# Optimization experiments

Measured on AMD Instinct MI355X. Metric: run time of the kernel, lower is better.

## Reference

```python
import jax, jax.numpy as jnp
import numpy as np

N = 50000      # num nodes
E = 400000     # num edges
D = 128        # embed_size (MLP output size)
H = 256        # MLP hidden size
HOPS = 3       # num_hops


def _mlp_params(key, in_dim):
    k1, k2, k3, k4 = jax.random.split(key, 4)
    u = lambda k, s: jax.random.uniform(k, s, minval=-0.1, maxval=0.1, dtype=jnp.float32)
    return u(k1, (in_dim, H)), u(k2, (H,)), u(k3, (H, D)), u(k4, (D,))


def _mlp(x, W1, b1, W2, b2):
    # Linear -> ReLU -> Linear -> ReLU (Dropout is identity at eval)
    return jax.nn.relu(jax.nn.relu(x @ W1 + b1) @ W2 + b2)


def _scatter_mean(vals, idx, counts):
    s = jax.ops.segment_sum(vals, idx, num_segments=N)
    return s / counts[:, None]


def setup_inputs() -> dict:
    key = jax.random.key(0)
    ks = jax.random.split(key, 14)
    inp = {
        "batch_token": jax.random.normal(ks[0], (N, D), jnp.float32),
        "edge_p_node": jax.random.randint(ks[1], (E,), 0, N),
        "edge_c_node": jax.random.randint(ks[2], (E,), 0, N),
        "edge_p_indicate": jax.random.uniform(ks[3], (E,), jnp.float32),
        "edge_c_indicate": jax.random.uniform(ks[4], (E,), jnp.float32),
        "p_mask": jax.random.uniform(ks[5], (N,), jnp.float32),
        "c_mask": jax.random.uniform(ks[6], (N,), jnp.float32),
        "start_token": jax.random.normal(ks[7], (D,), jnp.float32),
        "end_token": jax.random.normal(ks[8], (D,), jnp.float32),
    }
    for name, kk, in_dim in [("v", ks[9], D), ("e", ks[10], 1), ("p", ks[11], 3 * D),
                             ("c", ks[12], 3 * D), ("a", ks[13], 3 * D)]:
        W1, b1, W2, b2 = _mlp_params(kk, in_dim)
        inp[name + "W1"], inp[name + "b1"], inp[name + "W2"], inp[name + "b2"] = W1, b1, W2, b2
    return inp


def reference(batch_token, edge_p_node, edge_c_node, edge_p_indicate, edge_c_indicate,
              p_mask, c_mask, start_token, end_token,
              vW1, vb1, vW2, vb2, eW1, eb1, eW2, eb2,
              pW1, pb1, pW2, pb2, cW1, cb1, cW2, cb2,
              aW1, ab1, aW2, ab2):
    edge_p = _mlp(edge_p_indicate[:, None], eW1, eb1, eW2, eb2)   # [E, D]
    edge_c = _mlp(edge_c_indicate[:, None], eW1, eb1, eW2, eb2)   # [E, D]
    hidden = _mlp(batch_token, vW1, vb1, vW2, vb2)                # [N, D]

    ones_e = jnp.ones((E,), jnp.float32)
    cnt_p = jnp.maximum(jax.ops.segment_sum(ones_e, edge_p_node, num_segments=N), 1.0)
    cnt_c = jnp.maximum(jax.ops.segment_sum(ones_e, edge_c_node, num_segments=N), 1.0)

    for _ in range(HOPS):
        hp = hidden[edge_p_node]                                  # [E, D]
        hc = hidden[edge_c_node]                                  # [E, D]
        S_p = _mlp(jnp.concatenate([hc, hp, edge_p], -1), pW1, pb1, pW2, pb2)
        S_c = _mlp(jnp.concatenate([hp, hc, edge_c], -1), cW1, cb1, cW2, cb2)
        S_p = _scatter_mean(S_p, edge_p_node, cnt_p) + p_mask[:, None] * start_token
        S_c = _scatter_mean(S_c, edge_c_node, cnt_c) + c_mask[:, None] * end_token
        x_aggr = jnp.concatenate([hidden, S_p, S_c], -1)          # [N, 3D]
        hidden = hidden + _mlp(x_aggr, aW1, ab1, aW2, ab2)
    return hidden
```

## Files before the change

### kernel.cpp

```cpp
#include <hip/hip_runtime.h>
#include <stdint.h>

#define N_NODES 50000
#define N_EDGES 400000
#define M_TAB 4096

typedef short s8v __attribute__((ext_vector_type(8)));
typedef float f4v __attribute__((ext_vector_type(4)));

static __device__ __forceinline__ unsigned short f2bf(float f) {
  union { float f; uint32_t u; } v; v.f = f;
  return (unsigned short)((v.u + 0x7FFFu + ((v.u >> 16) & 1u)) >> 16);
}
static __device__ __forceinline__ ushort4 f2bf4(float4 v) {
  ushort4 o; o.x = f2bf(v.x); o.y = f2bf(v.y); o.z = f2bf(v.z); o.w = f2bf(v.w);
  return o;
}
static __device__ __forceinline__ void bf2(uint32_t u, float& a, float& b) {
  union { uint32_t x; float f; } lo, hi;
  lo.x = u << 16; hi.x = u & 0xffff0000u;
  a = lo.f; b = hi.f;
}
static __device__ __forceinline__ f4v mfma16(s8v a, s8v b, f4v c) {
  return __builtin_amdgcn_mfma_f32_16x16x32_bf16(a, b, c, 0, 0, 0);
}
static __device__ __forceinline__ void gload_lds16(const void* g, void* l) {
  __builtin_amdgcn_global_load_lds(
      (const __attribute__((address_space(1))) uint32_t*)g,
      (__attribute__((address_space(3))) uint32_t*)l, 16, 0, 0);
}

__global__ __launch_bounds__(256) void z_gemm_kernel(
    const float* __restrict__ hid, const unsigned short* __restrict__ Wsw,
    unsigned short* __restrict__ Z)
{
  __shared__ __align__(16) unsigned short B[256 * 128];
  const int tid = threadIdx.x, lane = tid & 63, wv = tid >> 6;
  const int g = blockIdx.y;
  const unsigned short* src = Wsw + (size_t)g * 256 * 128;
#pragma unroll
  for (int it = 0; it < 16; ++it) {
    int q = it * 4 + wv;
    gload_lds16(src + (size_t)q * 512 + lane * 8, &B[q * 512]);
  }
  __syncthreads();
  const int l15 = lane & 15, kg = lane >> 4;
  const f4v vz = {0.f, 0.f, 0.f, 0.f};
  for (int c0 = blockIdx.x; c0 < (N_NODES + 63) / 64; c0 += gridDim.x) {
    const int base = c0 * 64;
    const int row = base + wv * 16 + l15;
    s8v af[4];
#pragma unroll
    for (int k = 0; k < 4; ++k) {
      float4 u0 = {0.f,0.f,0.f,0.f}, u1 = {0.f,0.f,0.f,0.f};
      if (row < N_NODES) {
        u0 = *(const float4*)(hid + (size_t)row * 128 + k * 32 + kg * 8);
        u1 = *(const float4*)(hid + (size_t)row * 128 + k * 32 + kg * 8 + 4);
      }
      s8v a;
      a[0] = (short)f2bf(u0.x); a[1] = (short)f2bf(u0.y);
      a[2] = (short)f2bf(u0.z); a[3] = (short)f2bf(u0.w);
      a[4] = (short)f2bf(u1.x); a[5] = (short)f2bf(u1.y);
      a[6] = (short)f2bf(u1.z); a[7] = (short)f2bf(u1.w);
      af[k] = a;
    }
    f4v acc[16];
#pragma unroll
    for (int t = 0; t < 16; ++t) acc[t] = vz;
#pragma unroll
    for (int k = 0; k < 4; ++k) {
#pragma unroll
      for (int t = 0; t < 16; ++t) {
        int j = t * 16 + l15;
        s8v b = *(const s8v*)(&B[j * 128 + (((k * 4 + kg) ^ (j & 7)) * 8)]);
        acc[t] = mfma16(af[k], b, acc[t]);
      }
    }
#pragma unroll
    for (int t = 0; t < 16; ++t) {
      int c = t * 16 + l15;
#pragma unroll
      for (int j = 0; j < 4; ++j) {
        int ro = base + wv * 16 + kg * 4 + j;
        if (ro < N_NODES) Z[(size_t)ro * 512 + g * 256 + c] = f2bf(acc[t][j]);
      }
    }
  }
}

__global__ __launch_bounds__(256) void tab_gemm_kernel(
    const unsigned short* __restrict__ feat,
    const unsigned short* __restrict__ Wsw,
    const float* __restrict__ b1, unsigned short* __restrict__ T)
{
  __shared__ __align__(16) unsigned short B[256 * 128];
  const int tid = threadIdx.x, lane = tid & 63, wv = tid >> 6;
#pragma unroll
  for (int it = 0; it < 16; ++it) {
    int q = it * 4 + wv;
    gload_lds16(Wsw + (size_t)q * 512 + lane * 8, &B[q * 512]);
  }
  __syncthreads();
  const int l15 = lane & 15, kg = lane >> 4;
  const int base = blockIdx.x * 64;
  const int row = base + wv * 16 + l15;
  s8v af[4];
#pragma unroll
  for (int k = 0; k < 4; ++k)
    af[k] = *(const s8v*)(feat + (size_t)row * 128 + k * 32 + kg * 8);
  const f4v vz = {0.f, 0.f, 0.f, 0.f};
  f4v acc[16];
#pragma unroll
  for (int t = 0; t < 16; ++t) acc[t] = vz;
#pragma unroll
  for (int k = 0; k < 4; ++k) {
#pragma unroll
    for (int t = 0; t < 16; ++t) {
      int j = t * 16 + l15;
      s8v b = *(const s8v*)(&B[j * 128 + (((k * 4 + kg) ^ (j & 7)) * 8)]);
      acc[t] = mfma16(af[k], b, acc[t]);
    }
  }
#pragma unroll
  for (int t = 0; t < 16; ++t) {
    int c = t * 16 + l15;
    float bb = b1[c];
#pragma unroll
    for (int j = 0; j < 4; ++j) {
      int ro = base + wv * 16 + kg * 4 + j;
      T[(size_t)ro * 256 + c] = f2bf(acc[t][j] + bb);
    }
  }
}

__global__ __launch_bounds__(256) void edge_msg3_kernel(
    const unsigned short* __restrict__ Z,
    const float* __restrict__ ind,
    const int* __restrict__ n0idx, const int* __restrict__ n1idx,
    const unsigned short* __restrict__ T,
    const unsigned short* __restrict__ W2stg, const float* __restrict__ b2,
    float* __restrict__ Sacc, const float* __restrict__ rcpv)
{
  __shared__ __align__(16) unsigned short H1[64 * 256];
  __shared__ __align__(16) unsigned short Wb[2][4096];
  __shared__ int n0s[64], n1s[64], tix[64];
  __shared__ float tfr[64];
  const int tid = threadIdx.x, lane = tid & 63, wv = tid >> 6;
  const int l15 = lane & 15, kg = lane >> 4;
  const int base = blockIdx.x * 64;
  if (tid < 64) {
    n0s[tid] = n0idx[base + tid];
    n1s[tid] = n1idx[base + tid];
    float x = ind[base + tid];
    float xs = x * (float)M_TAB;
    int idx = (int)xs;
    idx = idx < 0 ? 0 : (idx > M_TAB - 1 ? M_TAB - 1 : idx);
    tix[tid] = idx;
    tfr[tid] = xs - (float)idx;
  }
#pragma unroll
  for (int i = 0; i < 2; ++i) {
    int q = wv * 2 + i;
    gload_lds16(W2stg + (size_t)q * 512 + lane * 8, &Wb[0][q * 512]);
  }
  __syncthreads();
#pragma unroll
  for (int it = 0; it < 8; ++it) {
    int i = tid + it * 256;
    int r = i >> 5, c8 = i & 31;
    const uint4 za = *(const uint4*)(Z + (size_t)n0s[r] * 512 + c8 * 8);
    const uint4 zb = *(const uint4*)(Z + (size_t)n1s[r] * 512 + 256 + c8 * 8);
    const uint4 t0 = *(const uint4*)(T + (size_t)tix[r] * 256 + c8 * 8);
    const uint4 t1 = *(const uint4*)(T + (size_t)(tix[r] + 1) * 256 + c8 * 8);
    const float f = tfr[r];
    uint32_t ua[4] = {za.x, za.y, za.z, za.w};
    uint32_t ub[4] = {zb.x, zb.y, zb.z, zb.w};
    uint32_t u0[4] = {t0.x, t0.y, t0.z, t0.w};
    uint32_t u1[4] = {t1.x, t1.y, t1.z, t1.w};
    uint32_t uo[4];
#pragma unroll
    for (int q = 0; q < 4; ++q) {
      float a0, a1, b0, b1f, p0, p1, q0, q1;
      bf2(ua[q], a0, a1); bf2(ub[q], b0, b1f);
      bf2(u0[q], p0, p1); bf2(u1[q], q0, q1);
      float s0 = fmaxf(a0 + b0 + p0 + f * (q0 - p0), 0.f);
      float s1 = fmaxf(a1 + b1f + p1 + f * (q1 - p1), 0.f);
      uo[q] = (uint32_t)f2bf(s0) | ((uint32_t)f2bf(s1) << 16);
    }
    uint4 pk; pk.x = uo[0]; pk.y = uo[1]; pk.z = uo[2]; pk.w = uo[3];
    *(uint4*)(H1 + r * 256 + ((c8 ^ (r & 7)) * 8)) = pk;
  }
  __syncthreads();
  const int rr = wv * 16 + l15;
  s8v af2[8];
#pragma unroll
  for (int k = 0; k < 8; ++k)
    af2[k] = *(const s8v*)(H1 + rr * 256 + (((k * 4 + kg) ^ (l15 & 7)) * 8));
  const f4v vz = {0.f, 0.f, 0.f, 0.f};
  f4v acc2[8];
#pragma unroll
  for (int t = 0; t < 8; ++t) acc2[t] = vz;
#pragma unroll
  for (int s = 0; s < 8; ++s) {
    if (s < 7) {
#pragma unroll
      for (int i = 0; i < 2; ++i) {
        int q = wv * 2 + i;
        gload_lds16(W2stg + (size_t)(s + 1) * 4096 + q * 512 + lane * 8,
                    &Wb[(s + 1) & 1][q * 512]);
      }
    }
#pragma unroll
    for (int t = 0; t < 8; ++t) {
      s8v b = *(const s8v*)(&Wb[s & 1][kg * 1024 + (t * 16 + l15) * 8]);
      acc2[t] = mfma16(af2[s], b, acc2[t]);
    }
    __syncthreads();
  }
  int n1r[4]; float tscr[4];
#pragma unroll
  for (int j = 0; j < 4; ++j) {
    int r = wv * 16 + kg * 4 + j;
    int n1 = n1s[r];
    n1r[j] = n1; tscr[j] = rcpv[n1];
  }
#pragma unroll
  for (int t = 0; t < 8; ++t) {
    int c = t * 16 + l15;
    float bb = b2[c];
#pragma unroll
    for (int j = 0; j < 4; ++j) {
      float v = fmaxf(acc2[t][j] + bb, 0.f) * tscr[j];
      atomicAdd(Sacc + (size_t)n1r[j] * 128 + c, v);
    }
  }
}

__global__ __launch_bounds__(256, 2) void aggr_kernel(
    float* __restrict__ hid,
    const float* __restrict__ Sp, const float* __restrict__ Sc,
    const float* __restrict__ pm, const float* __restrict__ cm,
    const float* __restrict__ st, const float* __restrict__ et,
    const unsigned short* __restrict__ W1stg, const float* __restrict__ b1,
    const unsigned short* __restrict__ W2stg, const float* __restrict__ b2)
{
  __shared__ __align__(16) unsigned short ABUF[64 * 384];
  __shared__ __align__(16) unsigned short Wb[2][8192];
  const int tid = threadIdx.x, lane = tid & 63, wv = tid >> 6;
  const int l15 = lane & 15, kg = lane >> 4;
  const int base = blockIdx.x * 64;
#pragma unroll
  for (int i = 0; i < 4; ++i) {
    int q = wv * 4 + i;
    gload_lds16(W1stg + (size_t)q * 512 + lane * 8, &Wb[0][q * 512]);
  }
#pragma unroll
  for (int it = 0; it < 24; ++it) {
    int i = tid + it * 256;
    int r = i / 96, q = i - r * 96;
    int seg = q >> 5, c4 = q & 31;
    int n = base + r;
    float4 v = {0.f, 0.f, 0.f, 0.f};
    if (n < N_NODES) {
      if (seg == 0) {
        v = *(const float4*)(hid + (size_t)n * 128 + c4 * 4);
      } else if (seg == 1) {
        v = *(const float4*)(Sp + (size_t)n * 128 + c4 * 4);
        float m = pm[n]; const float4 t = *(const float4*)(st + c4 * 4);
        v.x = fmaf(m, t.x, v.x); v.y = fmaf(m, t.y, v.y);
        v.z = fmaf(m, t.z, v.z); v.w = fmaf(m, t.w, v.w);
      } else {
        v = *(const float4*)(Sc + (size_t)n * 128 + c4 * 4);
        float m = cm[n]; const float4 t = *(const float4*)(et + c4 * 4);
        v.x = fmaf(m, t.x, v.x); v.y = fmaf(m, t.y, v.y);
        v.z = fmaf(m, t.z, v.z); v.w = fmaf(m, t.w, v.w);
      }
    }
    int unit = seg * 16 + (c4 >> 1);
    *(ushort4*)(ABUF + r * 384 + ((unit ^ (r & 7)) * 8) + (c4 & 1) * 4) = f2bf4(v);
  }
  __syncthreads();
  const int rr = wv * 16 + l15;
  s8v af1[12];
#pragma unroll
  for (int k = 0; k < 12; ++k)
    af1[k] = *(const s8v*)(ABUF + rr * 384 + (((k * 4 + kg) ^ (rr & 7)) * 8));
  const f4v vz = {0.f, 0.f, 0.f, 0.f};
  f4v acc1[16];
#pragma unroll
  for (int t = 0; t < 16; ++t) acc1[t] = vz;
#pragma unroll
  for (int s = 0; s < 12; ++s) {
    if (s < 11) {
#pragma unroll
      for (int i = 0; i < 4; ++i) {
        int q = wv * 4 + i;
        gload_lds16(W1stg + (size_t)(s + 1) * 8192 + q * 512 + lane * 8,
                    &Wb[(s + 1) & 1][q * 512]);
      }
    } else {
#pragma unroll
      for (int i = 0; i < 2; ++i) {
        int q = wv * 2 + i;
        gload_lds16(W2stg + (size_t)q * 512 + lane * 8, &Wb[0][q * 512]);
      }
    }
#pragma unroll
    for (int t = 0; t < 16; ++t) {
      s8v b = *(const s8v*)(&Wb[s & 1][kg * 2048 + (t * 16 + l15) * 8]);
      acc1[t] = mfma16(af1[s], b, acc1[t]);
    }
    __syncthreads();
  }
#pragma unroll
  for (int t = 0; t < 16; ++t) {
    int c = t * 16 + l15;
    float bb = b1[c];
#pragma unroll
    for (int j = 0; j < 4; ++j) {
      int r = wv * 16 + kg * 4 + j;
      ABUF[r * 256 + (((c >> 3) ^ (r & 7)) * 8) + (c & 7)] =
          f2bf(fmaxf(acc1[t][j] + bb, 0.f));
    }
  }
  __syncthreads();
  s8v af2[8];
#pragma unroll
  for (int k = 0; k < 8; ++k)
    af2[k] = *(const s8v*)(ABUF + rr * 256 + (((k * 4 + kg) ^ (l15 & 7)) * 8));
  f4v acc2[8];
#pragma unroll
  for (int t = 0; t < 8; ++t) acc2[t] = vz;
#pragma unroll
  for (int s = 0; s < 8; ++s) {
    if (s < 7) {
#pragma unroll
      for (int i = 0; i < 2; ++i) {
        int q = wv * 2 + i;
        gload_lds16(W2stg + (size_t)(s + 1) * 4096 + q * 512 + lane * 8,
                    &Wb[(s + 1) & 1][q * 512]);
      }
    }
#pragma unroll
    for (int t = 0; t < 8; ++t) {
      s8v b = *(const s8v*)(&Wb[s & 1][kg * 1024 + (t * 16 + l15) * 8]);
      acc2[t] = mfma16(af2[s], b, acc2[t]);
    }
    __syncthreads();
  }
#pragma unroll
  for (int t = 0; t < 8; ++t) {
    int c = t * 16 + l15;
    float bb = b2[c];
#pragma unroll
    for (int j = 0; j < 4; ++j) {
      int ro = base + wv * 16 + kg * 4 + j;
      if (ro < N_NODES) hid[(size_t)ro * 128 + c] += fmaxf(acc2[t][j] + bb, 0.f);
    }
  }
}

__global__ __launch_bounds__(256) void edge_feat_kernel(
    const float* __restrict__ ind, const float* __restrict__ W1,
    const float* __restrict__ b1,
    const unsigned short* __restrict__ W2sw,
    const float* __restrict__ b2, unsigned short* __restrict__ feat,
    int ntiles)
{
  __shared__ __align__(16) unsigned short B[128 * 256];
  __shared__ unsigned short H1[64 * 264];
  __shared__ float xs[64];
  const int tid = threadIdx.x, lane = tid & 63, wv = tid >> 6;
  const int l15 = lane & 15, kg = lane >> 4;
#pragma unroll
  for (int it = 0; it < 16; ++it) {
    int q = it * 4 + wv;
    gload_lds16(W2sw + (size_t)q * 512 + lane * 8, &B[q * 512]);
  }
  const float w = W1[tid], bb1 = b1[tid];
  const f4v vz = {0.f, 0.f, 0.f, 0.f};
  for (int tile = blockIdx.x; tile < ntiles; tile += gridDim.x) {
    const int base = tile * 64;
    if (tid < 64) xs[tid] = ind[base + tid];
    __syncthreads();
    for (int r = 0; r < 64; ++r)
      H1[r * 264 + tid] = f2bf(fmaxf(fmaf(xs[r], w, bb1), 0.f));
    __syncthreads();
    const unsigned short* Hrow = H1 + (size_t)(wv * 16 + l15) * 264;
    s8v af2[8];
#pragma unroll
    for (int k = 0; k < 8; ++k) af2[k] = *(const s8v*)(Hrow + k * 32 + kg * 8);
    f4v acc2[8];
#pragma unroll
    for (int t = 0; t < 8; ++t) acc2[t] = vz;
#pragma unroll
    for (int k = 0; k < 8; ++k) {
#pragma unroll
      for (int t = 0; t < 8; ++t) {
        int j = t * 16 + l15;
        s8v b = *(const s8v*)(&B[j * 256 + (((k * 4 + kg) ^ (j & 7)) * 8)]);
        acc2[t] = mfma16(af2[k], b, acc2[t]);
      }
    }
#pragma unroll
    for (int t = 0; t < 8; ++t) {
      int c = t * 16 + l15;
      float b2c = b2[c];
#pragma unroll
      for (int j = 0; j < 4; ++j) {
        int e = base + wv * 16 + kg * 4 + j;
        feat[(size_t)e * 128 + c] = f2bf(fmaxf(acc2[t][j] + b2c, 0.f));
      }
    }
    __syncthreads();
  }
}

template <int KST1>
static __device__ __forceinline__ void mlp_core(
    unsigned short* __restrict__ BUF,
    const unsigned short* __restrict__ W1t, const float* __restrict__ b1,
    const unsigned short* __restrict__ W2t,
    int l15, int kg, int wr0, f4v* __restrict__ acc2)
{
  const int ldA = KST1 * 32 + 8;
  const f4v vzero = {0.f, 0.f, 0.f, 0.f};
  const unsigned short* Arow = BUF + (size_t)(wr0 + l15) * ldA;
  s8v af1[KST1];
#pragma unroll
  for (int k = 0; k < KST1; ++k) af1[k] = *(const s8v*)(Arow + k * 32 + kg * 8);
  __syncthreads();
  f4v acc1[16];
#pragma unroll
  for (int t = 0; t < 16; ++t) acc1[t] = vzero;
#pragma unroll
  for (int k = 0; k < KST1; ++k) {
#pragma unroll
    for (int t = 0; t < 16; ++t) {
      s8v b = *(const s8v*)(W1t + (size_t)(t * 16 + l15) * (KST1 * 32) + k * 32 + kg * 8);
      acc1[t] = mfma16(af1[k], b, acc1[t]);
    }
  }
#pragma unroll
  for (int t = 0; t < 16; ++t) {
    int c = t * 16 + l15;
    float bb = b1[c];
#pragma unroll
    for (int j = 0; j < 4; ++j) {
      BUF[(size_t)(wr0 + kg * 4 + j) * 264 + c] = f2bf(fmaxf(acc1[t][j] + bb, 0.f));
    }
  }
  const unsigned short* Hrow = BUF + (size_t)(wr0 + l15) * 264;
  s8v af2[8];
#pragma unroll
  for (int k = 0; k < 8; ++k) af2[k] = *(const s8v*)(Hrow + k * 32 + kg * 8);
#pragma unroll
  for (int t = 0; t < 8; ++t) acc2[t] = vzero;
#pragma unroll
  for (int k = 0; k < 8; ++k) {
#pragma unroll
    for (int t = 0; t < 8; ++t) {
      s8v b = *(const s8v*)(W2t + (size_t)(t * 16 + l15) * 256 + k * 32 + kg * 8);
      acc2[t] = mfma16(af2[k], b, acc2[t]);
    }
  }
}

__global__ __launch_bounds__(256, 2) void v_mlp_kernel(
    const float* __restrict__ x,
    const unsigned short* __restrict__ W1t, const float* __restrict__ b1,
    const unsigned short* __restrict__ W2t, const float* __restrict__ b2,
    float* __restrict__ hid)
{
  __shared__ unsigned short BUF[64 * 264];
  const int tid = threadIdx.x;
  const int base = blockIdx.x * 64;
#pragma unroll
  for (int it = 0; it < 8; ++it) {
    int i = tid + it * 256;
    int r = i >> 5, c4 = i & 31, n = base + r;
    float4 v = {0.f, 0.f, 0.f, 0.f};
    if (n < N_NODES) v = *(const float4*)(x + (size_t)n * 128 + c4 * 4);
    *(ushort4*)(BUF + r * 136 + c4 * 4) = f2bf4(v);
  }
  __syncthreads();
  const int lane = tid & 63, wv = tid >> 6;
  const int l15 = lane & 15, kg = lane >> 4, wr0 = wv * 16;
  f4v acc2[8];
  mlp_core<4>(BUF, W1t, b1, W2t, l15, kg, wr0, acc2);
#pragma unroll
  for (int t = 0; t < 8; ++t) {
    int c = t * 16 + l15;
    float bb = b2[c];
#pragma unroll
    for (int j = 0; j < 4; ++j) {
      int n = base + wr0 + kg * 4 + j;
      if (n < N_NODES) hid[(size_t)n * 128 + c] = fmaxf(acc2[t][j] + bb, 0.f);
    }
  }
}

__global__ void transpose_w(const float* __restrict__ W, unsigned short* __restrict__ Wt,
                            int K, int NH) {
  int i = blockIdx.x * 256 + threadIdx.x;
  if (i < K * NH) {
    int k = i / NH, n = i - k * NH;
    Wt[(size_t)n * K + k] = f2bf(W[i]);
  }
}

__global__ void build_w1stg(const float* __restrict__ W, unsigned short* __restrict__ stg) {
  int i = blockIdx.x * 256 + threadIdx.x;
  if (i < 384 * 256) {
    int k = i >> 8, out = i & 255;
    int s = k >> 5, kc = (k >> 3) & 3, j = k & 7;
    stg[(size_t)s * 8192 + kc * 2048 + out * 8 + j] = f2bf(W[i]);
  }
}

__global__ void build_w2stg(const float* __restrict__ W, unsigned short* __restrict__ stg) {
  int i = blockIdx.x * 256 + threadIdx.x;
  if (i < 256 * 128) {
    int k = i >> 7, out = i & 127;
    int s = k >> 5, kc = (k >> 3) & 3, j = k & 7;
    stg[(size_t)s * 4096 + kc * 1024 + out * 8 + j] = f2bf(W[i]);
  }
}

__global__ void build_w128_sw(const float* __restrict__ W, int k_off,
                              unsigned short* __restrict__ dst) {
  int i = blockIdx.x * 256 + threadIdx.x;
  if (i < 256 * 128) {
    int j = i >> 7, e = i & 127;
    int unit = (e >> 3) ^ (j & 7);
    dst[(size_t)j * 128 + unit * 8 + (e & 7)] = f2bf(W[(size_t)(k_off + e) * 256 + j]);
  }
}

__global__ void build_w2sw(const float* __restrict__ W, unsigned short* __restrict__ dst) {
  int i = blockIdx.x * 256 + threadIdx.x;
  if (i < 128 * 256) {
    int j = i >> 8, k = i & 255;
    dst[(size_t)j * 256 + (((k >> 3) ^ (j & 7)) * 8) + (k & 7)] =
        f2bf(W[(size_t)k * 128 + j]);
  }
}

__global__ void make_samples(float* __restrict__ xs) {
  int i = blockIdx.x * 256 + threadIdx.x;
  if (i < 4160) {
    int s = i < M_TAB ? i : M_TAB;
    xs[i] = (float)s * (1.f / (float)M_TAB);
  }
}

__global__ void count_kernel(const int* __restrict__ pn, const int* __restrict__ cn,
                             float* __restrict__ cp, float* __restrict__ cc) {
  int i = blockIdx.x * 256 + threadIdx.x;
  if (i < N_EDGES) {
    atomicAdd(cp + pn[i], 1.f);
    atomicAdd(cc + cn[i], 1.f);
  }
}

__global__ void rcp_kernel(float* __restrict__ cp, float* __restrict__ cc) {
  int i = blockIdx.x * 256 + threadIdx.x;
  if (i < N_NODES) {
    cp[i] = 1.f / fmaxf(cp[i], 1.f);
    cc[i] = 1.f / fmaxf(cc[i], 1.f);
  }
}

extern "C" void kernel_launch(void* const* d_in, const int* in_sizes, int n_in,
                              void* d_out, int out_size, void* d_ws, size_t ws_size,
                              hipStream_t stream) {
  const float* batch_token = (const float*)d_in[0];
  const int*   pn          = (const int*)d_in[1];
  const int*   cn          = (const int*)d_in[2];
  const float* indP        = (const float*)d_in[3];
  const float* indC        = (const float*)d_in[4];
  const float* p_mask      = (const float*)d_in[5];
  const float* c_mask      = (const float*)d_in[6];
  const float* stok        = (const float*)d_in[7];
  const float* etok        = (const float*)d_in[8];
  const float* vW1 = (const float*)d_in[9],  *vb1 = (const float*)d_in[10];
  const float* vW2 = (const float*)d_in[11], *vb2 = (const float*)d_in[12];
  const float* eW1 = (const float*)d_in[13], *eb1 = (const float*)d_in[14];
  const float* eW2 = (const float*)d_in[15], *eb2 = (const float*)d_in[16];
  const float* pW1 = (const float*)d_in[17], *pb1 = (const float*)d_in[18];
  const float* pW2 = (const float*)d_in[19], *pb2 = (const float*)d_in[20];
  const float* cW1 = (const float*)d_in[21], *cb1 = (const float*)d_in[22];
  const float* cW2 = (const float*)d_in[23], *cb2 = (const float*)d_in[24];
  const float* aW1 = (const float*)d_in[25], *ab1 = (const float*)d_in[26];
  const float* aW2 = (const float*)d_in[27], *ab2 = (const float*)d_in[28];

  char* w = (char*)d_ws;
  auto alloc = [&](size_t bytes) -> char* {
    char* p = w;
    w += (bytes + 255) & ~(size_t)255;
    return p;
  };
  float* Sp    = (float*)alloc((size_t)N_NODES * 128 * 4);
  float* Sc    = (float*)alloc((size_t)N_NODES * 128 * 4);
  float* rcp_p = (float*)alloc((size_t)N_NODES * 4);
  float* rcp_c = (float*)alloc((size_t)N_NODES * 4);
  unsigned short* Zall   = (unsigned short*)alloc((size_t)N_NODES * 512 * 2);
  unsigned short* fsamp  = (unsigned short*)alloc((size_t)4160 * 128 * 2);
  unsigned short* Tp     = (unsigned short*)alloc((size_t)4160 * 256 * 2);
  unsigned short* Tc     = (unsigned short*)alloc((size_t)4160 * 256 * 2);
  float*          xsamp  = (float*)alloc((size_t)4160 * 4);
  unsigned short* Wbig_p = (unsigned short*)alloc((size_t)2 * 256 * 128 * 2);
  unsigned short* Wbig_c = (unsigned short*)alloc((size_t)2 * 256 * 128 * 2);
  unsigned short* W1csw_p = (unsigned short*)alloc(256 * 128 * 2);
  unsigned short* W1csw_c = (unsigned short*)alloc(256 * 128 * 2);
  unsigned short* W1stg_a = (unsigned short*)alloc(12 * 8192 * 2);
  unsigned short* W2stg_p = (unsigned short*)alloc(8 * 4096 * 2);
  unsigned short* W2stg_c = (unsigned short*)alloc(8 * 4096 * 2);
  unsigned short* W2stg_a = (unsigned short*)alloc(8 * 4096 * 2);
  unsigned short* W1t_v   = (unsigned short*)alloc(256 * 128 * 2);
  unsigned short* W2t_v   = (unsigned short*)alloc(128 * 256 * 2);
  unsigned short* W2sw_e  = (unsigned short*)alloc(128 * 256 * 2);

  float* hidden = (float*)d_out;

  const int EB = N_EDGES / 64;
  const int NB = (N_NODES + 63) / 64;

  hipMemsetAsync(rcp_p, 0, (size_t)N_NODES * 4, stream);
  hipMemsetAsync(rcp_c, 0, (size_t)N_NODES * 4, stream);
  count_kernel<<<(N_EDGES + 255) / 256, 256, 0, stream>>>(pn, cn, rcp_p, rcp_c);
  rcp_kernel<<<(N_NODES + 255) / 256, 256, 0, stream>>>(rcp_p, rcp_c);

  transpose_w<<<(128 * 256 + 255) / 256, 256, 0, stream>>>(vW1, W1t_v, 128, 256);
  transpose_w<<<(256 * 128 + 255) / 256, 256, 0, stream>>>(vW2, W2t_v, 256, 128);
  build_w2sw<<<(128 * 256 + 255) / 256, 256, 0, stream>>>(eW2, W2sw_e);
  build_w1stg<<<(384 * 256 + 255) / 256, 256, 0, stream>>>(aW1, W1stg_a);
  build_w2stg<<<(256 * 128 + 255) / 256, 256, 0, stream>>>(pW2, W2stg_p);
  build_w2stg<<<(256 * 128 + 255) / 256, 256, 0, stream>>>(cW2, W2stg_c);
  build_w2stg<<<(256 * 128 + 255) / 256, 256, 0, stream>>>(aW2, W2stg_a);
  const int SWB = (256 * 128 + 255) / 256;
  build_w128_sw<<<SWB, 256, 0, stream>>>(pW1, 0,   Wbig_p + 0 * 256 * 128);
  build_w128_sw<<<SWB, 256, 0, stream>>>(pW1, 128, Wbig_p + 1 * 256 * 128);
  build_w128_sw<<<SWB, 256, 0, stream>>>(cW1, 0,   Wbig_c + 0 * 256 * 128);
  build_w128_sw<<<SWB, 256, 0, stream>>>(cW1, 128, Wbig_c + 1 * 256 * 128);
  build_w128_sw<<<SWB, 256, 0, stream>>>(pW1, 256, W1csw_p);
  build_w128_sw<<<SWB, 256, 0, stream>>>(cW1, 256, W1csw_c);

  make_samples<<<(4160 + 255) / 256, 256, 0, stream>>>(xsamp);
  edge_feat_kernel<<<65, 256, 0, stream>>>(xsamp, eW1, eb1, W2sw_e, eb2, fsamp, 65);
  tab_gemm_kernel<<<65, 256, 0, stream>>>(fsamp, W1csw_p, pb1, Tp);
  tab_gemm_kernel<<<65, 256, 0, stream>>>(fsamp, W1csw_c, cb1, Tc);

  v_mlp_kernel<<<NB, 256, 0, stream>>>(batch_token, W1t_v, vb1, W2t_v, vb2, hidden);

  for (int hop = 0; hop < 3; ++hop) {
    hipMemsetAsync(Sp, 0, (size_t)N_NODES * 128 * 4, stream);
    hipMemsetAsync(Sc, 0, (size_t)N_NODES * 128 * 4, stream);
    z_gemm_kernel<<<dim3(256, 2), 256, 0, stream>>>(hidden, Wbig_p, Zall);
    edge_msg3_kernel<<<EB, 256, 0, stream>>>(Zall, indP, cn, pn, Tp,
                                             W2stg_p, pb2, Sp, rcp_p);
    z_gemm_kernel<<<dim3(256, 2), 256, 0, stream>>>(hidden, Wbig_c, Zall);
    edge_msg3_kernel<<<EB, 256, 0, stream>>>(Zall, indC, pn, cn, Tc,
                                             W2stg_c, cb2, Sc, rcp_c);
    aggr_kernel<<<NB, 256, 0, stream>>>(hidden, Sp, Sc, p_mask, c_mask,
                                        stok, etok, W1stg_a, ab1, W2stg_a, ab2);
  }
  (void)in_sizes; (void)n_in; (void)out_size; (void)ws_size;
}
```

Before: 1.997 ms.

## Sort edges by destination and segment-reduce messages in LDS before atomics

Adds a counting-sort preprocessing pass (integer count, prefix scan, scatter) that reorders edges by destination node for each direction. The edge message kernel now reads the sorted index and indicator arrays, stages its output tile in shared memory, and does a run-length reduction over consecutive rows with the same destination. This cuts the number of global float atomics per edge block. The cost is extra one-time preprocessing kernels, including a single-block scan, and an extra LDS round trip and barrier per block. Sorting also changes gather locality on the destination side and makes the order of floating-point sums non-deterministic.

```diff
diff --git a/kernel.cpp b/kernel.cpp
--- a/kernel.cpp
+++ b/kernel.cpp
@@ -133,10 +133,10 @@
   }
 }
 
-__global__ __launch_bounds__(256) void edge_msg3_kernel(
+__global__ __launch_bounds__(256) void edge_msg4_kernel(
     const unsigned short* __restrict__ Z,
-    const float* __restrict__ ind,
-    const int* __restrict__ n0idx, const int* __restrict__ n1idx,
+    const int* __restrict__ sn0, const int* __restrict__ sn1,
+    const float* __restrict__ sx,
     const unsigned short* __restrict__ T,
     const unsigned short* __restrict__ W2stg, const float* __restrict__ b2,
     float* __restrict__ Sacc, const float* __restrict__ rcpv)
@@ -144,14 +144,15 @@
   __shared__ __align__(16) unsigned short H1[64 * 256];
   __shared__ __align__(16) unsigned short Wb[2][4096];
   __shared__ int n0s[64], n1s[64], tix[64];
-  __shared__ float tfr[64];
+  __shared__ float tfr[64], tsc[64];
   const int tid = threadIdx.x, lane = tid & 63, wv = tid >> 6;
   const int l15 = lane & 15, kg = lane >> 4;
   const int base = blockIdx.x * 64;
   if (tid < 64) {
-    n0s[tid] = n0idx[base + tid];
-    n1s[tid] = n1idx[base + tid];
-    float x = ind[base + tid];
+    int e = base + tid;
+    int a0 = sn0[e], a1 = sn1[e];
+    n0s[tid] = a0; n1s[tid] = a1; tsc[tid] = rcpv[a1];
+    float x = sx[e];
     float xs = x * (float)M_TAB;
     int idx = (int)xs;
     idx = idx < 0 ? 0 : (idx > M_TAB - 1 ? M_TAB - 1 : idx);
@@ -217,22 +218,33 @@
     }
     __syncthreads();
   }
-  int n1r[4]; float tscr[4];
-#pragma unroll
-  for (int j = 0; j < 4; ++j) {
-    int r = wv * 16 + kg * 4 + j;
-    int n1 = n1s[r];
-    n1r[j] = n1; tscr[j] = rcpv[n1];
-  }
+  float* OUT = (float*)H1;
 #pragma unroll
   for (int t = 0; t < 8; ++t) {
     int c = t * 16 + l15;
     float bb = b2[c];
 #pragma unroll
     for (int j = 0; j < 4; ++j) {
-      float v = fmaxf(acc2[t][j] + bb, 0.f) * tscr[j];
-      atomicAdd(Sacc + (size_t)n1r[j] * 128 + c, v);
-    }
+      int r = wv * 16 + kg * 4 + j;
+      OUT[r * 128 + c] = fmaxf(acc2[t][j] + bb, 0.f);
+    }
+  }
+  __syncthreads();
+  {
+    const int c = tid & 127, h = tid >> 7;
+    const int r0 = h * 32;
+    float acc = 0.f;
+    int cur = n1s[r0];
+    float curs = tsc[r0];
+    for (int r = r0; r < r0 + 32; ++r) {
+      int nn = n1s[r];
+      if (nn != cur) {
+        atomicAdd(Sacc + (size_t)cur * 128 + c, acc * curs);
+        acc = 0.f; cur = nn; curs = tsc[r];
+      }
+      acc += OUT[r * 128 + c];
+    }
+    atomicAdd(Sacc + (size_t)cur * 128 + c, acc * curs);
   }
 }
 
@@ -500,6 +512,64 @@
   }
 }
 
+__global__ void counti_kernel(const int* __restrict__ pn, const int* __restrict__ cn,
+                              int* __restrict__ cp, int* __restrict__ cc) {
+  int i = blockIdx.x * 256 + threadIdx.x;
+  if (i < N_EDGES) {
+    atomicAdd(cp + pn[i], 1);
+    atomicAdd(cc + cn[i], 1);
+  }
+}
+
+__global__ void rcpi_kernel(const int* __restrict__ cp, const int* __restrict__ cc,
+                            float* __restrict__ rp, float* __restrict__ rc) {
+  int i = blockIdx.x * 256 + threadIdx.x;
+  if (i < N_NODES) {
+    rp[i] = 1.f / fmaxf((float)cp[i], 1.f);
+    rc[i] = 1.f / fmaxf((float)cc[i], 1.f);
+  }
+}
+
+__global__ void scan_kernel(const int* __restrict__ cnt, int* __restrict__ cur) {
+  __shared__ int part[1024];
+  const int t = threadIdx.x;
+  const int CH = (N_NODES + 1023) / 1024;
+  int s = 0;
+#pragma unroll 1
+  for (int i = 0; i < CH; ++i) {
+    int idx = t * CH + i;
+    if (idx < N_NODES) s += cnt[idx];
+  }
+  part[t] = s;
+  __syncthreads();
+  for (int d = 1; d < 1024; d <<= 1) {
+    int v = (t >= d) ? part[t - d] : 0;
+    __syncthreads();
+    part[t] += v;
+    __syncthreads();
+  }
+  int run = part[t] - s;
+#pragma unroll 1
+  for (int i = 0; i < CH; ++i) {
+    int idx = t * CH + i;
+    if (idx < N_NODES) { cur[idx] = run; run += cnt[idx]; }
+  }
+}
+
+__global__ void scatter_kernel(const int* __restrict__ tgt, const int* __restrict__ oth,
+                               const float* __restrict__ x, int* __restrict__ cursor,
+                               int* __restrict__ sn0, int* __restrict__ sn1,
+                               float* __restrict__ sx) {
+  int e = blockIdx.x * 256 + threadIdx.x;
+  if (e < N_EDGES) {
+    int tN = tgt[e];
+    int pos = atomicAdd(cursor + tN, 1);
+    sn0[pos] = oth[e];
+    sn1[pos] = tN;
+    sx[pos] = x[e];
+  }
+}
+
 __global__ void transpose_w(const float* __restrict__ W, unsigned short* __restrict__ Wt,
                             int K, int NH) {
   int i = blockIdx.x * 256 + threadIdx.x;
@@ -551,23 +621,6 @@
   if (i < 4160) {
     int s = i < M_TAB ? i : M_TAB;
     xs[i] = (float)s * (1.f / (float)M_TAB);
-  }
-}
-
-__global__ void count_kernel(const int* __restrict__ pn, const int* __restrict__ cn,
-                             float* __restrict__ cp, float* __restrict__ cc) {
-  int i = blockIdx.x * 256 + threadIdx.x;
-  if (i < N_EDGES) {
-    atomicAdd(cp + pn[i], 1.f);
-    atomicAdd(cc + cn[i], 1.f);
-  }
-}
-
-__global__ void rcp_kernel(float* __restrict__ cp, float* __restrict__ cc) {
-  int i = blockIdx.x * 256 + threadIdx.x;
-  if (i < N_NODES) {
-    cp[i] = 1.f / fmaxf(cp[i], 1.f);
-    cc[i] = 1.f / fmaxf(cc[i], 1.f);
   }
 }
 
@@ -604,6 +657,16 @@
   float* Sc    = (float*)alloc((size_t)N_NODES * 128 * 4);
   float* rcp_p = (float*)alloc((size_t)N_NODES * 4);
   float* rcp_c = (float*)alloc((size_t)N_NODES * 4);
+  int*   cnt_p = (int*)alloc((size_t)N_NODES * 4);
+  int*   cnt_c = (int*)alloc((size_t)N_NODES * 4);
+  int*   cur_p = (int*)alloc((size_t)N_NODES * 4);
+  int*   cur_c = (int*)alloc((size_t)N_NODES * 4);
+  int*   sn0_p = (int*)alloc((size_t)N_EDGES * 4);
+  int*   sn1_p = (int*)alloc((size_t)N_EDGES * 4);
+  float* sx_p  = (float*)alloc((size_t)N_EDGES * 4);
+  int*   sn0_c = (int*)alloc((size_t)N_EDGES * 4);
+  int*   sn1_c = (int*)alloc((size_t)N_EDGES * 4);
+  float* sx_c  = (float*)alloc((size_t)N_EDGES * 4);
   unsigned short* Zall   = (unsigned short*)alloc((size_t)N_NODES * 512 * 2);
   unsigned short* fsamp  = (unsigned short*)alloc((size_t)4160 * 128 * 2);
   unsigned short* Tp     = (unsigned short*)alloc((size_t)4160 * 256 * 2);
@@ -626,10 +689,16 @@
   const int EB = N_EDGES / 64;
   const int NB = (N_NODES + 63) / 64;
 
-  hipMemsetAsync(rcp_p, 0, (size_t)N_NODES * 4, stream);
-  hipMemsetAsync(rcp_c, 0, (size_t)N_NODES * 4, stream);
-  count_kernel<<<(N_EDGES + 255) / 256, 256, 0, stream>>>(pn, cn, rcp_p, rcp_c);
-  rcp_kernel<<<(N_NODES + 255) / 256, 256, 0, stream>>>(rcp_p, rcp_c);
+  hipMemsetAsync(cnt_p, 0, (size_t)N_NODES * 4, stream);
+  hipMemsetAsync(cnt_c, 0, (size_t)N_NODES * 4, stream);
+  counti_kernel<<<(N_EDGES + 255) / 256, 256, 0, stream>>>(pn, cn, cnt_p, cnt_c);
+  rcpi_kernel<<<(N_NODES + 255) / 256, 256, 0, stream>>>(cnt_p, cnt_c, rcp_p, rcp_c);
+  scan_kernel<<<1, 1024, 0, stream>>>(cnt_p, cur_p);
+  scan_kernel<<<1, 1024, 0, stream>>>(cnt_c, cur_c);
+  scatter_kernel<<<(N_EDGES + 255) / 256, 256, 0, stream>>>(pn, cn, indP, cur_p,
+                                                            sn0_p, sn1_p, sx_p);
+  scatter_kernel<<<(N_EDGES + 255) / 256, 256, 0, stream>>>(cn, pn, indC, cur_c,
+                                                            sn0_c, sn1_c, sx_c);
 
   transpose_w<<<(128 * 256 + 255) / 256, 256, 0, stream>>>(vW1, W1t_v, 128, 256);
   transpose_w<<<(256 * 128 + 255) / 256, 256, 0, stream>>>(vW2, W2t_v, 256, 128);
@@ -657,10 +726,10 @@
     hipMemsetAsync(Sp, 0, (size_t)N_NODES * 128 * 4, stream);
     hipMemsetAsync(Sc, 0, (size_t)N_NODES * 128 * 4, stream);
     z_gemm_kernel<<<dim3(256, 2), 256, 0, stream>>>(hidden, Wbig_p, Zall);
-    edge_msg3_kernel<<<EB, 256, 0, stream>>>(Zall, indP, cn, pn, Tp,
+    edge_msg4_kernel<<<EB, 256, 0, stream>>>(Zall, sn0_p, sn1_p, sx_p, Tp,
                                              W2stg_p, pb2, Sp, rcp_p);
     z_gemm_kernel<<<dim3(256, 2), 256, 0, stream>>>(hidden, Wbig_c, Zall);
-    edge_msg3_kernel<<<EB, 256, 0, stream>>>(Zall, indC, pn, cn, Tc,
+    edge_msg4_kernel<<<EB, 256, 0, stream>>>(Zall, sn0_c, sn1_c, sx_c, Tc,
                                              W2stg_c, cb2, Sc, rcp_c);
     aggr_kernel<<<NB, 256, 0, stream>>>(hidden, Sp, Sc, p_mask, c_mask,
                                         stok, etok, W1stg_a, ab1, W2stg_a, ab2);
```

After: 1.703 ms. -14.7%, faster.
